# Kernel tuning notes

Hardware: AMD Instinct MI355X
Metric: run time of the kernel (lower is better)

Reference implementation:

```python
import jax, jax.numpy as jnp
import numpy as np

HIDDEN = 2880
N_HEADS = 64
N_KV_HEADS = 8
HEAD_DIM = 64
ROPE_THETA = 150000.0


def _rope(x, position_ids):
    # x: [B, H, S, D]; rotate-half RoPE as in the flax module
    inv_freq = 1.0 / (ROPE_THETA ** (jnp.arange(0, HEAD_DIM, 2, dtype=jnp.float32) / HEAD_DIM))
    b, h, s, d = x.shape
    freqs = jnp.outer(position_ids.reshape(-1).astype(jnp.float32), inv_freq)  # [B*S, D/2]
    cos = jnp.cos(freqs).reshape(b, 1, s, d // 2)
    sin = jnp.sin(freqs).reshape(b, 1, s, d // 2)
    x1, x2 = jnp.split(x, 2, axis=-1)
    return jnp.concatenate([x1 * cos - x2 * sin, x1 * sin + x2 * cos], axis=-1)


def setup_inputs() -> dict:
    key = jax.random.key(0)
    ks = jax.random.split(key, 5)
    B, S = 2, 1024
    x = jax.random.normal(ks[0], (B, S, HIDDEN), dtype=jnp.float32)
    wq = jax.random.normal(ks[1], (HIDDEN, N_HEADS * HEAD_DIM), dtype=jnp.float32) * 0.02
    wk = jax.random.normal(ks[2], (HIDDEN, N_KV_HEADS * HEAD_DIM), dtype=jnp.float32) * 0.02
    wv = jax.random.normal(ks[3], (HIDDEN, N_KV_HEADS * HEAD_DIM), dtype=jnp.float32) * 0.02
    wo = jax.random.normal(ks[4], (N_HEADS * HEAD_DIM, HIDDEN), dtype=jnp.float32) * 0.02
    position_ids = jnp.broadcast_to(jnp.arange(S, dtype=jnp.int32)[None, :], (B, S))
    return {"x": x, "wq": wq, "wk": wk, "wv": wv, "wo": wo, "position_ids": position_ids}


def reference(x, wq, wk, wv, wo, position_ids):
    b, s, _ = x.shape
    scale = 1.0 / np.sqrt(HEAD_DIM)
    q = (x @ wq).reshape(b, s, N_HEADS, HEAD_DIM).transpose(0, 2, 1, 3)       # [B,H,S,D]
    k = (x @ wk).reshape(b, s, N_KV_HEADS, HEAD_DIM).transpose(0, 2, 1, 3)    # [B,Hkv,S,D]
    v = (x @ wv).reshape(b, s, N_KV_HEADS, HEAD_DIM).transpose(0, 2, 1, 3)
    q = _rope(q, position_ids)
    k = _rope(k, position_ids)
    rep = N_HEADS // N_KV_HEADS
    k = jnp.repeat(k, rep, axis=1)  # GQA head-repeat as in original
    v = jnp.repeat(v, rep, axis=1)
    scores = jnp.einsum('bhqd,bhkd->bhqk', q, k) * scale
    causal = jnp.tril(jnp.ones((s, s), dtype=bool))[None, None, :, :]
    scores = jnp.where(causal, scores, -jnp.inf)
    probs = jax.nn.softmax(scores, axis=-1)
    out = jnp.einsum('bhqk,bhkd->bhqd', probs, v)
    out = out.transpose(0, 2, 1, 3).reshape(b, s, N_HEADS * HEAD_DIM)
    return out @ wo
```

## Files before the change

### kernel.cpp

```cpp
#include <hip/hip_runtime.h>

#define BB 2
#define SS 1024
#define HIDDEN 2880
#define NH 64
#define NKV 8
#define HD 64
#define M_TOK 2048
#define NQ 4096
#define NKVD 512
#define NQKV 5120
#define NOUT 2880
#define NOUT_PAD 2944

typedef __attribute__((ext_vector_type(8))) short short8;
typedef __attribute__((ext_vector_type(4))) float f32x4;

__device__ __forceinline__ unsigned short f2b(float x) {
  union { float f; unsigned u; } v; v.f = x;
  unsigned r = (v.u + 0x7FFFu + ((v.u >> 16) & 1u)) >> 16;
  return (unsigned short)r;
}

__device__ __forceinline__ void gload16(const void* g, void* l) {
  __builtin_amdgcn_global_load_lds(
      (const __attribute__((address_space(1))) void*)g,
      (__attribute__((address_space(3))) void*)l, 16, 0, 0);
}

__global__ __launch_bounds__(256) void cast_x_kernel(const float* __restrict__ in,
                                                     unsigned short* __restrict__ out,
                                                     int n4) {
  int idx = blockIdx.x * 256 + threadIdx.x;
  if (idx >= n4) return;
  float4 v = ((const float4*)in)[idx];
  ushort4 o;
  o.x = f2b(v.x); o.y = f2b(v.y); o.z = f2b(v.z); o.w = f2b(v.w);
  ((ushort4*)out)[idx] = o;
}

__global__ __launch_bounds__(256) void transpose_cast(const float* __restrict__ in,
                                                      long ldin,
                                                      unsigned short* __restrict__ out,
                                                      int K, int N) {
  __shared__ float t[32][33];
  const int n0 = blockIdx.x * 32, k0 = blockIdx.y * 32;
  const int tx = threadIdx.x, ty = threadIdx.y;
#pragma unroll
  for (int i = 0; i < 4; ++i) {
    int k = k0 + ty + i * 8;
    int n = n0 + tx;
    t[ty + i * 8][tx] = (n < N) ? in[(long)k * ldin + n] : 0.f;
  }
  __syncthreads();
#pragma unroll
  for (int i = 0; i < 4; ++i) {
    int n = n0 + ty + i * 8;
    int k = k0 + tx;
    out[(long)n * K + k] = f2b(t[tx][ty + i * 8]);
  }
}

__global__ __launch_bounds__(256) void rope_table(const int* __restrict__ pos,
                                                  float* __restrict__ ct,
                                                  float* __restrict__ st) {
  int tid = blockIdx.x * 256 + threadIdx.x;
  int t = tid >> 5, i = tid & 31;
  float p = (float)pos[t];
  float f = p * expf(-(float)i * (11.918390573078392f / 32.f));
  ct[tid] = cosf(f);
  st[tid] = sinf(f);
}

__global__ __launch_bounds__(256) void rope_q_pack(const float* __restrict__ qkvf,
                                                   const float* __restrict__ ct,
                                                   const float* __restrict__ st,
                                                   unsigned short* __restrict__ qb) {
  int tid = blockIdx.x * 256 + threadIdx.x;
  int i = tid & 31;
  int h = (tid >> 5) & 63;
  int t = tid >> 11;
  const float* src = qkvf + (size_t)t * NQKV + h * 64;
  float x1 = src[i], x2 = src[i + 32];
  float c = ct[t * 32 + i], s = st[t * 32 + i];
  int b = t >> 10, sidx = t & 1023;
  unsigned short* dst = qb + (((size_t)(b * NH + h)) * SS + sidx) * HD;
  dst[i]      = f2b((x1 * c - x2 * s) * 0.125f);
  dst[i + 32] = f2b((x1 * s + x2 * c) * 0.125f);
}

__global__ __launch_bounds__(256) void rope_k_pack(const float* __restrict__ qkvf,
                                                   const float* __restrict__ ct,
                                                   const float* __restrict__ st,
                                                   unsigned short* __restrict__ kb) {
  int tid = blockIdx.x * 256 + threadIdx.x;
  int i = tid & 31;
  int h = (tid >> 5) & 7;
  int t = tid >> 8;
  const float* src = qkvf + (size_t)t * NQKV + NQ + h * 64;
  float x1 = src[i], x2 = src[i + 32];
  float c = ct[t * 32 + i], s = st[t * 32 + i];
  int b = t >> 10, sidx = t & 1023;
  unsigned short* dst = kb + (((size_t)(b * NKV + h)) * SS + sidx) * HD;
  dst[i]      = f2b(x1 * c - x2 * s);
  dst[i + 32] = f2b(x1 * s + x2 * c);
}

__global__ __launch_bounds__(256, 3) void gemm128(const unsigned short* __restrict__ A,
                                                  const unsigned short* __restrict__ Bt,
                                                  float* __restrict__ C,
                                                  int lda, int ldc, int Nvalid) {
  __shared__ char lA[128 * 128];
  __shared__ char lB[128 * 128];
  const int tid = threadIdx.x;
  const int lane = tid & 63;
  const int w = tid >> 6;
  const int m16 = lane & 15, g4 = lane >> 4;
  const int wr = w >> 1, wc = w & 1;
  const int bm = blockIdx.y * 128, bn = blockIdx.x * 128;
  const size_t strb = (size_t)lda * 2;

  const int srow = tid >> 3;
  const int scolb = ((tid & 7) * 16) ^ ((srow & 7) << 4);
  const int sdst = w * 1024;
  const char* ga0 = (const char*)A + (size_t)(bm + srow) * strb + scolb;
  const char* gb0 = (const char*)Bt + (size_t)(bn + srow) * strb + scolb;

  const int swz = (m16 & 7) << 4;
  const int kc0 = (g4 * 16) ^ swz;
  const int kc1 = (64 + g4 * 16) ^ swz;

  f32x4 acc[4][4];
#pragma unroll
  for (int i = 0; i < 4; ++i)
#pragma unroll
    for (int j = 0; j < 4; ++j) acc[i][j] = (f32x4){0.f, 0.f, 0.f, 0.f};

  const int NT = lda >> 6;
  for (int t = 0; t < NT; ++t) {
    const size_t ko = (size_t)t * 128;
    __syncthreads();
#pragma unroll
    for (int i = 0; i < 4; ++i) {
      gload16(ga0 + (size_t)(i * 32) * strb + ko, lA + i * 4096 + sdst);
      gload16(gb0 + (size_t)(i * 32) * strb + ko, lB + i * 4096 + sdst);
    }
    __syncthreads();
    short8 af[4][2], bf[4][2];
#pragma unroll
    for (int mq = 0; mq < 4; ++mq) {
      const int row = wr * 64 + mq * 16 + m16;
      af[mq][0] = *(const short8*)(lA + row * 128 + kc0);
      af[mq][1] = *(const short8*)(lA + row * 128 + kc1);
    }
#pragma unroll
    for (int nf = 0; nf < 4; ++nf) {
      const int row = wc * 64 + nf * 16 + m16;
      bf[nf][0] = *(const short8*)(lB + row * 128 + kc0);
      bf[nf][1] = *(const short8*)(lB + row * 128 + kc1);
    }
    __builtin_amdgcn_s_setprio(1);
#pragma unroll
    for (int mq = 0; mq < 4; ++mq)
#pragma unroll
      for (int nf = 0; nf < 4; ++nf) {
        acc[mq][nf] = __builtin_amdgcn_mfma_f32_16x16x32_bf16(af[mq][0], bf[nf][0], acc[mq][nf], 0, 0, 0);
        acc[mq][nf] = __builtin_amdgcn_mfma_f32_16x16x32_bf16(af[mq][1], bf[nf][1], acc[mq][nf], 0, 0, 0);
      }
    __builtin_amdgcn_s_setprio(0);
  }

#pragma unroll
  for (int mq = 0; mq < 4; ++mq) {
    const size_t row = bm + wr * 64 + mq * 16 + g4 * 4;
#pragma unroll
    for (int nf = 0; nf < 4; ++nf) {
      const int col = bn + wc * 64 + nf * 16 + m16;
      if (col < Nvalid) {
#pragma unroll
        for (int r = 0; r < 4; ++r)
          C[(row + r) * (size_t)ldc + col] = acc[mq][nf][r];
      }
    }
  }
}

__global__ __launch_bounds__(512) void attn_fwd(const unsigned short* __restrict__ qb,
                                                const unsigned short* __restrict__ kb,
                                                const unsigned short* __restrict__ vtb,
                                                unsigned short* __restrict__ ao) {
  __shared__ unsigned short kB[2][64 * 64];
  __shared__ unsigned short vB[2][64 * 64];
  __shared__ unsigned short pB[8][32 * 64];
  const int tid = threadIdx.x, lane = tid & 63, w = tid >> 6;
  const int qblk = blockIdx.x;
  const int bh = blockIdx.y;
  const int b = bh >> 6, h = bh & 63, hkv = h >> 3;
  const int m16 = lane & 15, g4 = lane >> 4;
  const int rbase = qblk * 256 + w * 32;

  const unsigned short* qp =
      qb + (((size_t)(b * NH + h)) * SS + rbase + m16) * HD + g4 * 8;
  const short8 q00 = *(const short8*)(qp);
  const short8 q01 = *(const short8*)(qp + 32);
  const short8 q10 = *(const short8*)(qp + 16 * HD);
  const short8 q11 = *(const short8*)(qp + 16 * HD + 32);

  const char* kbp = (const char*)(kb + ((size_t)(b * NKV + hkv)) * SS * HD);
  const char* vbp = (const char*)(vtb + ((size_t)(b * NKV + hkv)) * HD * SS);

  const int lrow = lane >> 3;
  const int lcolb = ((lane & 7) * 16) ^ ((lrow & 7) << 4);
  unsigned short* kDst0 = &kB[0][w * 512];
  unsigned short* kDst1 = &kB[1][w * 512];
  unsigned short* vDst0 = &vB[0][w * 512];
  unsigned short* vDst1 = &vB[1][w * 512];
  const size_t kRowOff = (size_t)(w * 8 + lrow) * 128 + lcolb;
  const size_t vRowOff = (size_t)(w * 8 + lrow) * 2048 + lcolb;

  const short8 ones = {(short)0x3F80, (short)0x3F80, (short)0x3F80, (short)0x3F80,
                       (short)0x3F80, (short)0x3F80, (short)0x3F80, (short)0x3F80};

  f32x4 o0[4], o1[4];
#pragma unroll
  for (int n = 0; n < 4; ++n) { o0[n] = (f32x4){0,0,0,0}; o1[n] = (f32x4){0,0,0,0}; }
  f32x4 lacc0 = (f32x4){0,0,0,0}, lacc1 = (f32x4){0,0,0,0};
  float mrow0[4] = {-1e30f,-1e30f,-1e30f,-1e30f};
  float mrow1[4] = {-1e30f,-1e30f,-1e30f,-1e30f};

  char* pw = (char*)pB[w];
  const int swz_m = (m16 & 7) << 4;
  const int nt = (qblk + 1) * 4;

  gload16(kbp + kRowOff, kDst0);
  gload16(vbp + vRowOff, vDst0);
  __syncthreads();

  for (int t = 0; t < nt; ++t) {
    const int k0 = t * 64;
    const char* kLds = (const char*)kB[t & 1];
    const char* vLds = (const char*)vB[t & 1];
    if (t + 1 < nt) {
      if (t & 1) { gload16(kbp + (size_t)(t + 1) * 8192 + kRowOff, kDst0);
                   gload16(vbp + (size_t)(t + 1) * 128  + vRowOff, vDst0); }
      else       { gload16(kbp + (size_t)(t + 1) * 8192 + kRowOff, kDst1);
                   gload16(vbp + (size_t)(t + 1) * 128  + vRowOff, vDst1); }
    }
    if (k0 < rbase + 32) {
      short8 kf0[4], kf1[4];
#pragma unroll
      for (int kf = 0; kf < 4; ++kf) {
        const int rb = (kf * 16 + m16) * 128;
        kf0[kf] = *(const short8*)(kLds + ((rb + g4 * 16) ^ swz_m));
        kf1[kf] = *(const short8*)(kLds + ((rb + 64 + g4 * 16) ^ swz_m));
      }
      f32x4 s0[4], s1[4];
      __builtin_amdgcn_s_setprio(1);
#pragma unroll
      for (int kf = 0; kf < 4; ++kf) {
        f32x4 z = (f32x4){0,0,0,0};
        z = __builtin_amdgcn_mfma_f32_16x16x32_bf16(q00, kf0[kf], z, 0, 0, 0);
        z = __builtin_amdgcn_mfma_f32_16x16x32_bf16(q01, kf1[kf], z, 0, 0, 0);
        s0[kf] = z;
        f32x4 z2 = (f32x4){0,0,0,0};
        z2 = __builtin_amdgcn_mfma_f32_16x16x32_bf16(q10, kf0[kf], z2, 0, 0, 0);
        z2 = __builtin_amdgcn_mfma_f32_16x16x32_bf16(q11, kf1[kf], z2, 0, 0, 0);
        s1[kf] = z2;
      }
      __builtin_amdgcn_s_setprio(0);
      if (k0 + 63 >= rbase) {
#pragma unroll
        for (int kf = 0; kf < 4; ++kf)
#pragma unroll
          for (int r = 0; r < 4; ++r) {
            const int col = k0 + kf * 16 + m16;
            if (col > rbase + g4 * 4 + r)      s0[kf][r] = -1e30f;
            if (col > rbase + 16 + g4 * 4 + r) s1[kf][r] = -1e30f;
          }
      }
      int grow = 0;
#pragma unroll
      for (int kf = 0; kf < 4; ++kf)
#pragma unroll
        for (int r = 0; r < 4; ++r) {
          grow |= (s0[kf][r] > mrow0[r] + 8.f);
          grow |= (s1[kf][r] > mrow1[r] + 8.f);
        }
      if (__any(grow)) {
        float mx0[4], mx1[4];
#pragma unroll
        for (int r = 0; r < 4; ++r) {
          mx0[r] = fmaxf(fmaxf(s0[0][r], s0[1][r]), fmaxf(s0[2][r], s0[3][r]));
          mx1[r] = fmaxf(fmaxf(s1[0][r], s1[1][r]), fmaxf(s1[2][r], s1[3][r]));
        }
#pragma unroll
        for (int off = 1; off <= 8; off <<= 1)
#pragma unroll
          for (int r = 0; r < 4; ++r) {
            mx0[r] = fmaxf(mx0[r], __shfl_xor(mx0[r], off));
            mx1[r] = fmaxf(mx1[r], __shfl_xor(mx1[r], off));
          }
#pragma unroll
        for (int r = 0; r < 4; ++r) {
          float mn0 = fmaxf(mrow0[r], mx0[r]);
          float sc0 = __expf(mrow0[r] - mn0);
          mrow0[r] = mn0; lacc0[r] *= sc0;
          float mn1 = fmaxf(mrow1[r], mx1[r]);
          float sc1 = __expf(mrow1[r] - mn1);
          mrow1[r] = mn1; lacc1[r] *= sc1;
#pragma unroll
          for (int n = 0; n < 4; ++n) { o0[n][r] *= sc0; o1[n][r] *= sc1; }
        }
      }
#pragma unroll
      for (int kf = 0; kf < 4; ++kf)
#pragma unroll
        for (int r = 0; r < 4; ++r) {
          const int colb = (kf * 16 + m16) * 2;
          int row = g4 * 4 + r;
          *(unsigned short*)(pw + ((row * 128 + colb) ^ ((row & 7) << 4))) =
              f2b(__expf(s0[kf][r] - mrow0[r]));
          row += 16;
          *(unsigned short*)(pw + ((row * 128 + colb) ^ ((row & 7) << 4))) =
              f2b(__expf(s1[kf][r] - mrow1[r]));
        }
      const int prb0 = m16 * 128, prb1 = (16 + m16) * 128;
      short8 pf00 = *(const short8*)(pw + ((prb0 + g4 * 16) ^ swz_m));
      short8 pf01 = *(const short8*)(pw + ((prb0 + 64 + g4 * 16) ^ swz_m));
      short8 pf10 = *(const short8*)(pw + ((prb1 + g4 * 16) ^ swz_m));
      short8 pf11 = *(const short8*)(pw + ((prb1 + 64 + g4 * 16) ^ swz_m));
      __builtin_amdgcn_s_setprio(1);
      lacc0 = __builtin_amdgcn_mfma_f32_16x16x32_bf16(pf00, ones, lacc0, 0, 0, 0);
      lacc0 = __builtin_amdgcn_mfma_f32_16x16x32_bf16(pf01, ones, lacc0, 0, 0, 0);
      lacc1 = __builtin_amdgcn_mfma_f32_16x16x32_bf16(pf10, ones, lacc1, 0, 0, 0);
      lacc1 = __builtin_amdgcn_mfma_f32_16x16x32_bf16(pf11, ones, lacc1, 0, 0, 0);
#pragma unroll
      for (int n = 0; n < 4; ++n) {
        const int rb = (n * 16 + m16) * 128;
        short8 vf0 = *(const short8*)(vLds + ((rb + g4 * 16) ^ swz_m));
        short8 vf1 = *(const short8*)(vLds + ((rb + 64 + g4 * 16) ^ swz_m));
        o0[n] = __builtin_amdgcn_mfma_f32_16x16x32_bf16(pf00, vf0, o0[n], 0, 0, 0);
        o0[n] = __builtin_amdgcn_mfma_f32_16x16x32_bf16(pf01, vf1, o0[n], 0, 0, 0);
        o1[n] = __builtin_amdgcn_mfma_f32_16x16x32_bf16(pf10, vf0, o1[n], 0, 0, 0);
        o1[n] = __builtin_amdgcn_mfma_f32_16x16x32_bf16(pf11, vf1, o1[n], 0, 0, 0);
      }
      __builtin_amdgcn_s_setprio(0);
    }
    __syncthreads();
  }

  float inv0[4], inv1[4];
#pragma unroll
  for (int r = 0; r < 4; ++r) { inv0[r] = 1.f / lacc0[r]; inv1[r] = 1.f / lacc1[r]; }
  const size_t row0 = (size_t)b * SS + rbase + g4 * 4;
#pragma unroll
  for (int n = 0; n < 4; ++n)
#pragma unroll
    for (int r = 0; r < 4; ++r) {
      ao[(row0 + r) * (size_t)NQ + h * 64 + n * 16 + m16] = f2b(o0[n][r] * inv0[r]);
      ao[(row0 + 16 + r) * (size_t)NQ + h * 64 + n * 16 + m16] = f2b(o1[n][r] * inv1[r]);
    }
}

constexpr size_t OFF_XB    = 0;
constexpr size_t OFF_WQKVT = 11796480;
constexpr size_t OFF_WOT   = 41287680;
constexpr size_t OFF_COS   = 65404928;
constexpr size_t OFF_SIN   = 65667072;
constexpr size_t OFF_QKVF  = 65929216;
constexpr size_t OFF_QB    = 107872256;
constexpr size_t OFF_KB    = 124649472;
constexpr size_t OFF_VTB   = 126746624;

extern "C" void kernel_launch(void* const* d_in, const int* in_sizes, int n_in,
                              void* d_out, int out_size, void* d_ws, size_t ws_size,
                              hipStream_t stream) {
  const float* x  = (const float*)d_in[0];
  const float* wq = (const float*)d_in[1];
  const float* wk = (const float*)d_in[2];
  const float* wv = (const float*)d_in[3];
  const float* wo = (const float*)d_in[4];
  const int* pos  = (const int*)d_in[5];
  float* out = (float*)d_out;
  char* ws = (char*)d_ws;

  unsigned short* xb    = (unsigned short*)(ws + OFF_XB);
  unsigned short* wqkvt = (unsigned short*)(ws + OFF_WQKVT);
  unsigned short* wot   = (unsigned short*)(ws + OFF_WOT);
  float* ct             = (float*)(ws + OFF_COS);
  float* st             = (float*)(ws + OFF_SIN);
  float* qkvf           = (float*)(ws + OFF_QKVF);
  unsigned short* qbuf  = (unsigned short*)(ws + OFF_QB);
  unsigned short* kbuf  = (unsigned short*)(ws + OFF_KB);
  unsigned short* vtb   = (unsigned short*)(ws + OFF_VTB);
  unsigned short* attnb = (unsigned short*)(ws + OFF_QKVF);

  cast_x_kernel<<<(M_TOK * HIDDEN / 4 + 255) / 256, 256, 0, stream>>>(x, xb, M_TOK * HIDDEN / 4);
  rope_table<<<(M_TOK * 32) / 256, 256, 0, stream>>>(pos, ct, st);
  transpose_cast<<<dim3(NQ / 32, HIDDEN / 32), dim3(32, 8), 0, stream>>>(
      wq, NQ, wqkvt, HIDDEN, NQ);
  transpose_cast<<<dim3(NKVD / 32, HIDDEN / 32), dim3(32, 8), 0, stream>>>(
      wk, NKVD, wqkvt + (size_t)NQ * HIDDEN, HIDDEN, NKVD);
  transpose_cast<<<dim3(NKVD / 32, HIDDEN / 32), dim3(32, 8), 0, stream>>>(
      wv, NKVD, wqkvt + (size_t)(NQ + NKVD) * HIDDEN, HIDDEN, NKVD);
  transpose_cast<<<dim3(NOUT_PAD / 32, NQ / 32), dim3(32, 8), 0, stream>>>(
      wo, NOUT, wot, NQ, NOUT);
  gemm128<<<dim3(NQKV / 128, M_TOK / 128), 256, 0, stream>>>(
      xb, wqkvt, qkvf, HIDDEN, NQKV, NQKV);
  rope_q_pack<<<(M_TOK * NH * 32) / 256, 256, 0, stream>>>(qkvf, ct, st, qbuf);
  rope_k_pack<<<(M_TOK * NKV * 32) / 256, 256, 0, stream>>>(qkvf, ct, st, kbuf);
  for (int b = 0; b < BB; ++b)
    transpose_cast<<<dim3(NKVD / 32, SS / 32), dim3(32, 8), 0, stream>>>(
        qkvf + (size_t)b * SS * NQKV + (NQ + NKVD), NQKV,
        vtb + (size_t)b * NKVD * SS, SS, NKVD);
  attn_fwd<<<dim3(4, BB * NH), 512, 0, stream>>>(qbuf, kbuf, vtb, attnb);
  gemm128<<<dim3(NOUT_PAD / 128, M_TOK / 128), 256, 0, stream>>>(
      attnb, wot, out, NQ, NOUT, NOUT);
}
```

Baseline: 271.3 us.

## Fuse RoPE, Q/K packing and V transpose into the QKV GEMM epilogue

The QKV projection GEMM now applies RoPE and writes bf16 Q/K in head-major layout, and V transposed, directly from its accumulators. This removes the fp32 QKV intermediate buffer and the separate rope_q_pack, rope_k_pack and V transpose launches. The cost is an epilogue with scattered 2-byte stores, most visibly the V transpose writes strided by SS. Each wave's 64-column slice maps to exactly one head, so the rotate-half pairs sit inside the wave's own accumulators.

New measurement: 256.7 us. 5.4% less time.

```diff
diff --git a/kernel.cpp b/kernel.cpp
--- a/kernel.cpp
+++ b/kernel.cpp
@@ -72,104 +72,61 @@
   st[tid] = sinf(f);
 }
 
-__global__ __launch_bounds__(256) void rope_q_pack(const float* __restrict__ qkvf,
-                                                   const float* __restrict__ ct,
-                                                   const float* __restrict__ st,
-                                                   unsigned short* __restrict__ qb) {
-  int tid = blockIdx.x * 256 + threadIdx.x;
-  int i = tid & 31;
-  int h = (tid >> 5) & 63;
-  int t = tid >> 11;
-  const float* src = qkvf + (size_t)t * NQKV + h * 64;
-  float x1 = src[i], x2 = src[i + 32];
-  float c = ct[t * 32 + i], s = st[t * 32 + i];
-  int b = t >> 10, sidx = t & 1023;
-  unsigned short* dst = qb + (((size_t)(b * NH + h)) * SS + sidx) * HD;
-  dst[i]      = f2b((x1 * c - x2 * s) * 0.125f);
-  dst[i + 32] = f2b((x1 * s + x2 * c) * 0.125f);
-}
-
-__global__ __launch_bounds__(256) void rope_k_pack(const float* __restrict__ qkvf,
-                                                   const float* __restrict__ ct,
-                                                   const float* __restrict__ st,
-                                                   unsigned short* __restrict__ kb) {
-  int tid = blockIdx.x * 256 + threadIdx.x;
-  int i = tid & 31;
-  int h = (tid >> 5) & 7;
-  int t = tid >> 8;
-  const float* src = qkvf + (size_t)t * NQKV + NQ + h * 64;
-  float x1 = src[i], x2 = src[i + 32];
-  float c = ct[t * 32 + i], s = st[t * 32 + i];
-  int b = t >> 10, sidx = t & 1023;
-  unsigned short* dst = kb + (((size_t)(b * NKV + h)) * SS + sidx) * HD;
-  dst[i]      = f2b(x1 * c - x2 * s);
-  dst[i + 32] = f2b(x1 * s + x2 * c);
-}
+#define GEMM128_BODY(Aptr, Bptr, lda)                                                     \
+  __shared__ char lA[128 * 128];                                                          \
+  __shared__ char lB[128 * 128];                                                          \
+  const int tid = threadIdx.x;                                                            \
+  const int lane = tid & 63;                                                              \
+  const int w = tid >> 6;                                                                 \
+  const int m16 = lane & 15, g4 = lane >> 4;                                              \
+  const int wr = w >> 1, wc = w & 1;                                                      \
+  const int bm = blockIdx.y * 128, bn = blockIdx.x * 128;                                 \
+  const size_t strb = (size_t)(lda) * 2;                                                  \
+  const int srow = tid >> 3;                                                              \
+  const int scolb = ((tid & 7) * 16) ^ ((srow & 7) << 4);                                 \
+  const int sdst = w * 1024;                                                              \
+  const char* ga0 = (const char*)(Aptr) + (size_t)(bm + srow) * strb + scolb;             \
+  const char* gb0 = (const char*)(Bptr) + (size_t)(bn + srow) * strb + scolb;             \
+  const int swz = (m16 & 7) << 4;                                                         \
+  const int kc0 = (g4 * 16) ^ swz;                                                        \
+  const int kc1 = (64 + g4 * 16) ^ swz;                                                   \
+  f32x4 acc[4][4];                                                                        \
+  _Pragma("unroll") for (int i = 0; i < 4; ++i)                                           \
+  _Pragma("unroll") for (int j = 0; j < 4; ++j) acc[i][j] = (f32x4){0.f, 0.f, 0.f, 0.f};  \
+  const int NT = (lda) >> 6;                                                              \
+  for (int t = 0; t < NT; ++t) {                                                          \
+    const size_t ko = (size_t)t * 128;                                                    \
+    __syncthreads();                                                                      \
+    _Pragma("unroll") for (int i = 0; i < 4; ++i) {                                       \
+      gload16(ga0 + (size_t)(i * 32) * strb + ko, lA + i * 4096 + sdst);                  \
+      gload16(gb0 + (size_t)(i * 32) * strb + ko, lB + i * 4096 + sdst);                  \
+    }                                                                                     \
+    __syncthreads();                                                                      \
+    short8 af[4][2], bf[4][2];                                                            \
+    _Pragma("unroll") for (int mq = 0; mq < 4; ++mq) {                                    \
+      const int row = wr * 64 + mq * 16 + m16;                                            \
+      af[mq][0] = *(const short8*)(lA + row * 128 + kc0);                                 \
+      af[mq][1] = *(const short8*)(lA + row * 128 + kc1);                                 \
+    }                                                                                     \
+    _Pragma("unroll") for (int nf = 0; nf < 4; ++nf) {                                    \
+      const int row = wc * 64 + nf * 16 + m16;                                            \
+      bf[nf][0] = *(const short8*)(lB + row * 128 + kc0);                                 \
+      bf[nf][1] = *(const short8*)(lB + row * 128 + kc1);                                 \
+    }                                                                                     \
+    __builtin_amdgcn_s_setprio(1);                                                        \
+    _Pragma("unroll") for (int mq = 0; mq < 4; ++mq)                                      \
+    _Pragma("unroll") for (int nf = 0; nf < 4; ++nf) {                                    \
+      acc[mq][nf] = __builtin_amdgcn_mfma_f32_16x16x32_bf16(af[mq][0], bf[nf][0], acc[mq][nf], 0, 0, 0); \
+      acc[mq][nf] = __builtin_amdgcn_mfma_f32_16x16x32_bf16(af[mq][1], bf[nf][1], acc[mq][nf], 0, 0, 0); \
+    }                                                                                     \
+    __builtin_amdgcn_s_setprio(0);                                                        \
+  }
 
 __global__ __launch_bounds__(256, 3) void gemm128(const unsigned short* __restrict__ A,
                                                   const unsigned short* __restrict__ Bt,
                                                   float* __restrict__ C,
                                                   int lda, int ldc, int Nvalid) {
-  __shared__ char lA[128 * 128];
-  __shared__ char lB[128 * 128];
-  const int tid = threadIdx.x;
-  const int lane = tid & 63;
-  const int w = tid >> 6;
-  const int m16 = lane & 15, g4 = lane >> 4;
-  const int wr = w >> 1, wc = w & 1;
-  const int bm = blockIdx.y * 128, bn = blockIdx.x * 128;
-  const size_t strb = (size_t)lda * 2;
-
-  const int srow = tid >> 3;
-  const int scolb = ((tid & 7) * 16) ^ ((srow & 7) << 4);
-  const int sdst = w * 1024;
-  const char* ga0 = (const char*)A + (size_t)(bm + srow) * strb + scolb;
-  const char* gb0 = (const char*)Bt + (size_t)(bn + srow) * strb + scolb;
-
-  const int swz = (m16 & 7) << 4;
-  const int kc0 = (g4 * 16) ^ swz;
-  const int kc1 = (64 + g4 * 16) ^ swz;
-
-  f32x4 acc[4][4];
-#pragma unroll
-  for (int i = 0; i < 4; ++i)
-#pragma unroll
-    for (int j = 0; j < 4; ++j) acc[i][j] = (f32x4){0.f, 0.f, 0.f, 0.f};
-
-  const int NT = lda >> 6;
-  for (int t = 0; t < NT; ++t) {
-    const size_t ko = (size_t)t * 128;
-    __syncthreads();
-#pragma unroll
-    for (int i = 0; i < 4; ++i) {
-      gload16(ga0 + (size_t)(i * 32) * strb + ko, lA + i * 4096 + sdst);
-      gload16(gb0 + (size_t)(i * 32) * strb + ko, lB + i * 4096 + sdst);
-    }
-    __syncthreads();
-    short8 af[4][2], bf[4][2];
-#pragma unroll
-    for (int mq = 0; mq < 4; ++mq) {
-      const int row = wr * 64 + mq * 16 + m16;
-      af[mq][0] = *(const short8*)(lA + row * 128 + kc0);
-      af[mq][1] = *(const short8*)(lA + row * 128 + kc1);
-    }
-#pragma unroll
-    for (int nf = 0; nf < 4; ++nf) {
-      const int row = wc * 64 + nf * 16 + m16;
-      bf[nf][0] = *(const short8*)(lB + row * 128 + kc0);
-      bf[nf][1] = *(const short8*)(lB + row * 128 + kc1);
-    }
-    __builtin_amdgcn_s_setprio(1);
-#pragma unroll
-    for (int mq = 0; mq < 4; ++mq)
-#pragma unroll
-      for (int nf = 0; nf < 4; ++nf) {
-        acc[mq][nf] = __builtin_amdgcn_mfma_f32_16x16x32_bf16(af[mq][0], bf[nf][0], acc[mq][nf], 0, 0, 0);
-        acc[mq][nf] = __builtin_amdgcn_mfma_f32_16x16x32_bf16(af[mq][1], bf[nf][1], acc[mq][nf], 0, 0, 0);
-      }
-    __builtin_amdgcn_s_setprio(0);
-  }
-
+  GEMM128_BODY(A, Bt, lda)
 #pragma unroll
   for (int mq = 0; mq < 4; ++mq) {
     const size_t row = bm + wr * 64 + mq * 16 + g4 * 4;
@@ -180,6 +137,57 @@
 #pragma unroll
         for (int r = 0; r < 4; ++r)
           C[(row + r) * (size_t)ldc + col] = acc[mq][nf][r];
+      }
+    }
+  }
+}
+
+__global__ __launch_bounds__(256, 3) void gemm128_qkv(const unsigned short* __restrict__ A,
+                                                      const unsigned short* __restrict__ Bt,
+                                                      const float* __restrict__ ct,
+                                                      const float* __restrict__ st,
+                                                      unsigned short* __restrict__ qb,
+                                                      unsigned short* __restrict__ kb,
+                                                      unsigned short* __restrict__ vtb,
+                                                      int lda) {
+  GEMM128_BODY(A, Bt, lda)
+  const int region = (bn < 4096) ? 0 : ((bn < 4608) ? 1 : 2);
+#pragma unroll
+  for (int mq = 0; mq < 4; ++mq) {
+    const int row = bm + wr * 64 + mq * 16 + g4 * 4;
+    if (region == 2) {
+#pragma unroll
+      for (int nf = 0; nf < 4; ++nf) {
+        const int d = (bn - 4608) + wc * 64 + nf * 16 + m16;
+#pragma unroll
+        for (int r = 0; r < 4; ++r) {
+          const int t = row + r;
+          const int b = t >> 10, sidx = t & 1023;
+          vtb[((size_t)(b * NKVD + d)) * SS + sidx] = f2b(acc[mq][nf][r]);
+        }
+      }
+    } else {
+#pragma unroll
+      for (int nf = 0; nf < 2; ++nf) {
+        const int i = nf * 16 + m16;
+#pragma unroll
+        for (int r = 0; r < 4; ++r) {
+          const int t = row + r;
+          const int b = t >> 10, sidx = t & 1023;
+          const float x1 = acc[mq][nf][r], x2 = acc[mq][nf + 2][r];
+          const float c = ct[t * 32 + i], s = st[t * 32 + i];
+          if (region == 0) {
+            const int h = (bn >> 6) + wc;
+            unsigned short* dst = qb + (((size_t)(b * NH + h)) * SS + sidx) * HD;
+            dst[i]      = f2b((x1 * c - x2 * s) * 0.125f);
+            dst[i + 32] = f2b((x1 * s + x2 * c) * 0.125f);
+          } else {
+            const int hk = ((bn - 4096) >> 6) + wc;
+            unsigned short* dst = kb + (((size_t)(b * NKV + hk)) * SS + sidx) * HD;
+            dst[i]      = f2b(x1 * c - x2 * s);
+            dst[i + 32] = f2b(x1 * s + x2 * c);
+          }
+        }
       }
     }
   }
@@ -367,10 +375,10 @@
 constexpr size_t OFF_WOT   = 41287680;
 constexpr size_t OFF_COS   = 65404928;
 constexpr size_t OFF_SIN   = 65667072;
-constexpr size_t OFF_QKVF  = 65929216;
-constexpr size_t OFF_QB    = 107872256;
-constexpr size_t OFF_KB    = 124649472;
-constexpr size_t OFF_VTB   = 126746624;
+constexpr size_t OFF_QB    = 65929216;
+constexpr size_t OFF_KB    = 82706432;
+constexpr size_t OFF_VTB   = 84803584;
+constexpr size_t OFF_ATTNB = 86900736;
 
 extern "C" void kernel_launch(void* const* d_in, const int* in_sizes, int n_in,
                               void* d_out, int out_size, void* d_ws, size_t ws_size,
@@ -389,11 +397,10 @@
   unsigned short* wot   = (unsigned short*)(ws + OFF_WOT);
   float* ct             = (float*)(ws + OFF_COS);
   float* st             = (float*)(ws + OFF_SIN);
-  float* qkvf           = (float*)(ws + OFF_QKVF);
   unsigned short* qbuf  = (unsigned short*)(ws + OFF_QB);
   unsigned short* kbuf  = (unsigned short*)(ws + OFF_KB);
   unsigned short* vtb   = (unsigned short*)(ws + OFF_VTB);
-  unsigned short* attnb = (unsigned short*)(ws + OFF_QKVF);
+  unsigned short* attnb = (unsigned short*)(ws + OFF_ATTNB);
 
   cast_x_kernel<<<(M_TOK * HIDDEN / 4 + 255) / 256, 256, 0, stream>>>(x, xb, M_TOK * HIDDEN / 4);
   rope_table<<<(M_TOK * 32) / 256, 256, 0, stream>>>(pos, ct, st);
@@ -405,14 +412,8 @@
       wv, NKVD, wqkvt + (size_t)(NQ + NKVD) * HIDDEN, HIDDEN, NKVD);
   transpose_cast<<<dim3(NOUT_PAD / 32, NQ / 32), dim3(32, 8), 0, stream>>>(
       wo, NOUT, wot, NQ, NOUT);
-  gemm128<<<dim3(NQKV / 128, M_TOK / 128), 256, 0, stream>>>(
-      xb, wqkvt, qkvf, HIDDEN, NQKV, NQKV);
-  rope_q_pack<<<(M_TOK * NH * 32) / 256, 256, 0, stream>>>(qkvf, ct, st, qbuf);
-  rope_k_pack<<<(M_TOK * NKV * 32) / 256, 256, 0, stream>>>(qkvf, ct, st, kbuf);
-  for (int b = 0; b < BB; ++b)
-    transpose_cast<<<dim3(NKVD / 32, SS / 32), dim3(32, 8), 0, stream>>>(
-        qkvf + (size_t)b * SS * NQKV + (NQ + NKVD), NQKV,
-        vtb + (size_t)b * NKVD * SS, SS, NKVD);
+  gemm128_qkv<<<dim3(NQKV / 128, M_TOK / 128), 256, 0, stream>>>(
+      xb, wqkvt, ct, st, qbuf, kbuf, vtb, HIDDEN);
   attn_fwd<<<dim3(4, BB * NH), 512, 0, stream>>>(qbuf, kbuf, vtb, attnb);
   gemm128<<<dim3(NOUT_PAD / 128, M_TOK / 128), 256, 0, stream>>>(
       attnb, wot, out, NQ, NOUT, NOUT);
```
